# Performance work log

Hardware: AMD Instinct MI355X
Metric: run time of the kernel (lower is better)

Reference implementation:

```python
import jax, jax.numpy as jnp
import numpy as np

PROJ_DIM = 128
TEMP = 0.1
CLAMP_VAL = 50.0
EPS = 1e-6


def _coords(H, W):
    # [H*W, 2] grid of (x, y) coordinates, matching torch meshgrid indexing='ij'
    xs = jnp.arange(W, dtype=jnp.float32)
    ys = jnp.arange(H, dtype=jnp.float32)
    grid_y, grid_x = jnp.meshgrid(ys, xs, indexing='ij')
    return jnp.stack([grid_x.reshape(-1), grid_y.reshape(-1)], axis=-1)


def setup_inputs() -> dict:
    key = jax.random.key(0)
    k1, k2 = jax.random.split(key)
    B, C, H, W = 2, 128, 96, 96
    fL = jax.random.normal(k1, (B, C, H, W), dtype=jnp.float32)
    fR = jax.random.normal(k2, (B, C, H, W), dtype=jnp.float32)
    return {"fL": fL, "fR": fR}


def reference(fL, fR):
    B, C, H, W = fL.shape
    HW = H * W
    scale = jnp.float32(np.sqrt(PROJ_DIM))

    # L2-normalize over channel dim with epsilon clamp
    fLn = fL / jnp.maximum(jnp.linalg.norm(fL, axis=1, keepdims=True), EPS)
    fRn = fR / jnp.maximum(jnp.linalg.norm(fR, axis=1, keepdims=True), EPS)

    q = fLn.reshape(B, C, HW).transpose(0, 2, 1).astype(jnp.float32)  # [B, HW, C]
    k = fRn.reshape(B, C, HW).astype(jnp.float32)                      # [B, C, HW]

    coords = _coords(H, W)  # [HW, 2]

    # Global correlation: [B, HW, HW] (chunking in the original is math-equivalent)
    corr = jnp.einsum('bqc,bck->bqk', q, k) / scale
    corr = jnp.clip(corr / TEMP, -CLAMP_VAL, CLAMP_VAL)
    prob = jax.nn.softmax(corr, axis=-1)

    expected_pos = prob @ coords                 # [B, HW, 2]
    max_prob = jnp.max(prob, axis=-1)            # [B, HW]

    flow_abs = expected_pos.reshape(B, H, W, 2).transpose(0, 3, 1, 2)  # [B, 2, H, W]
    conf = max_prob.reshape(B, 1, H, W)

    src = coords.reshape(H, W, 2).transpose(2, 0, 1)[None]  # [1, 2, H, W]
    flow = (flow_abs - src).astype(fL.dtype)
    conf = conf.astype(fL.dtype)
    return flow, conf
```

## Files before the change

kernel.cpp:

```cpp
#include <hip/hip_runtime.h>
#include <stdint.h>

#define HW 9216
#define CDIM 128
#define WIDTH 96
#define BATCH 2
#define SPLITS 48
#define KSPLIT 192
#define NKG 6
#define QTILE 128
#define NQT (HW / QTILE)
#define NWG (NQT * SPLITS * BATCH)

#define QSCALE 0.44194173824159216f
#define MXSCALE 2.8853900817779268f

typedef _Float16 half8 __attribute__((ext_vector_type(8)));
typedef float f32x16 __attribute__((ext_vector_type(16)));
typedef float float2v __attribute__((ext_vector_type(2)));

__global__ __launch_bounds__(256) void norm_kernel(const float* __restrict__ fL,
                                                   const float* __restrict__ fR,
                                                   _Float16* __restrict__ Qh,
                                                   _Float16* __restrict__ Kh)
{
    __shared__ float ssred[4][64];
    __shared__ _Float16 ot[64 * 130];

    const float* src = (blockIdx.y == 0) ? fL : fR;
    _Float16* dst    = (blockIdx.y == 0) ? Qh : Kh;
    const float outScale = (blockIdx.y == 0) ? QSCALE : 1.0f;

    const int t = threadIdx.x;
    const int pos_l = t & 63, cg = t >> 6;
    const int pos0 = blockIdx.x * 64;
    const int b = pos0 / HW, pos_in = pos0 % HW + pos_l;

    const float* p = src + (size_t)b * CDIM * HW + pos_in;

    float v[32];
    float ss = 0.f;
    #pragma unroll
    for (int j = 0; j < 32; ++j) {
        v[j] = p[(size_t)(cg * 32 + j) * HW];
        ss += v[j] * v[j];
    }
    ssred[cg][pos_l] = ss;
    __syncthreads();
    float tot = ssred[0][pos_l] + ssred[1][pos_l] + ssred[2][pos_l] + ssred[3][pos_l];
    float scale = outScale / fmaxf(sqrtf(tot), 1e-6f);

    #pragma unroll
    for (int j = 0; j < 32; ++j)
        ot[pos_l * 130 + cg * 32 + j] = (_Float16)(v[j] * scale);
    __syncthreads();

    uint4* og = (uint4*)(dst + (size_t)(b * HW + pos0 % HW + 0) * CDIM);
    #pragma unroll
    for (int i = 0; i < 4; ++i) {
        int idx = i * 256 + t;
        int row = idx >> 4, chunk = idx & 15;
        og[idx] = *(const uint4*)&ot[row * 130 + chunk * 8];
    }
}

__global__ __launch_bounds__(256, 3) void attn_kernel(const _Float16* __restrict__ Qh,
                                                      const _Float16* __restrict__ Kh,
                                                      float4* __restrict__ part)
{
    __shared__ __align__(16) _Float16 Ks[KSPLIT * 128];

    const int wg0 = blockIdx.x;
    const int nid = (wg0 & 7) * (NWG / 8) + (wg0 >> 3);
    const int qt = nid % NQT;
    const int sb = nid / NQT;
    const int split = sb % SPLITS;
    const int b = sb / SPLITS;

    const int t = threadIdx.x;
    const int lane = t & 63, wave = t >> 6;
    const int lane31 = lane & 31, hi = lane >> 5;
    const int ln15 = lane & 15, qd = lane >> 4;

    const char* kp0 = (const char*)(Kh + (size_t)b * HW * CDIM) +
                      (size_t)(split * KSPLIT) * (CDIM * 2);

    {
        int voff4[4];
        #pragma unroll
        for (int i = 0; i < 4; ++i) {
            int r = wave * 48 + i * 4 + qd;
            voff4[i] = r * 256 + ((ln15 ^ (r & 15)) << 4) - i * 1024;
        }
        _Float16* db = &Ks[wave * (48 * 128)];
        #pragma unroll
        for (int i = 0; i < 12; ++i)
            __builtin_amdgcn_global_load_lds(
                (const __attribute__((address_space(1))) uint32_t*)(kp0 + voff4[i & 3] + i * 1024),
                (__attribute__((address_space(3))) uint32_t*)(db + i * 512),
                16, 0, 0);
    }

    half8 qf[8];
    {
        const char* qb = (const char*)(Qh +
            ((size_t)(b * HW + qt * QTILE + wave * 32 + lane31)) * CDIM);
        #pragma unroll
        for (int kc = 0; kc < 8; ++kc)
            qf[kc] = *(const half8*)(qb + kc * 32 + hi * 16);
    }

    int rdoff[8];
    #pragma unroll
    for (int kc = 0; kc < 8; ++kc)
        rdoff[kc] = (lane31 << 8) + ((((kc << 1) | hi) ^ ln15) << 4);

    const float ysp = (float)(split * 2);

    float2v E2[8];
    #pragma unroll
    for (int p = 0; p < 8; ++p) E2[p] = (float2v)0.f;
    float mxs = -1.0e30f;
    float2v axb2 = (float2v)0.f, ay2 = (float2v)0.f;

    const char* ksb = (const char*)&Ks[0];
    const float2v C4 = (float2v)(1.0f / 24.0f), C3 = (float2v)(1.0f / 6.0f),
                  C2 = (float2v)0.5f, C1 = (float2v)1.0f;

    __syncthreads();

    #define CHAIN2(ACCX, KGX, ACCY, KGY)                                         \
        {                                                                        \
            __builtin_amdgcn_s_setprio(1);                                       \
            _Pragma("unroll")                                                    \
            for (int kc = 0; kc < 8; ++kc) {                                     \
                half8 kx = *(const half8*)(ksb + (KGX) * 8192 + rdoff[kc]);      \
                half8 ky = *(const half8*)(ksb + (KGY) * 8192 + rdoff[kc]);      \
                ACCX = __builtin_amdgcn_mfma_f32_32x32x16_f16(                   \
                    kx, qf[kc], (kc == 0) ? (f32x16)0.f : ACCX, 0, 0, 0);        \
                ACCY = __builtin_amdgcn_mfma_f32_32x32x16_f16(                   \
                    ky, qf[kc], (kc == 0) ? (f32x16)0.f : ACCY, 0, 0, 0);        \
            }                                                                    \
            __builtin_amdgcn_s_setprio(0);                                       \
        }

    #define EPI(ACC, KG)                                                         \
        {                                                                        \
            const float xb = (float)(32 * ((KG) % 3));                           \
            const float yk = ysp + (float)((KG) / 3);                            \
            float2v lt2;                                                         \
            _Pragma("unroll")                                                    \
            for (int p = 0; p < 8; ++p) {                                        \
                float2v w;                                                       \
                w.x = ACC[2 * p];                                                \
                w.y = ACC[2 * p + 1];                                            \
                mxs = fmaxf(mxs, fmaxf(w.x, w.y));           \
                float2v h = w * C4 + C3;                       \
                h = h * w + C2;                                                  \
                h = h * w + C1;                                                  \
                h = h * w + C1;                                                  \
                float2v e = h * h;                                               \
                E2[p] += e;                                                      \
                lt2 = (p == 0) ? e : (lt2 + e);                                  \
            }                                                                    \
            axb2 += lt2 * (float2v)xb;                                           \
            ay2  += lt2 * (float2v)yk;                                           \
        }

    f32x16 accA, accB, accC, accD;
    CHAIN2(accA, 0, accB, 1)
    CHAIN2(accC, 2, accD, 3)
    __builtin_amdgcn_sched_barrier(0); EPI(accA, 0) EPI(accB, 1)
    CHAIN2(accA, 4, accB, 5)
    __builtin_amdgcn_sched_barrier(0); EPI(accC, 2) EPI(accD, 3)
    EPI(accA, 4) EPI(accB, 5)
    #undef CHAIN2
    #undef EPI

    float l = 0.f, axc = 0.f;
    #pragma unroll
    for (int p = 0; p < 8; ++p) {
        const float c0 = (float)(((2 * p) & 3) + 8 * ((2 * p) >> 2));
        l   += E2[p].x + E2[p].y;
        axc += c0 * E2[p].x + (c0 + 1.0f) * E2[p].y;
    }
    float ax = axc + (float)(4 * hi) * l + axb2.x + axb2.y;
    float ay = ay2.x + ay2.y;
    float mx = mxs;

    l  += __shfl_xor(l, 32, 64);
    ax += __shfl_xor(ax, 32, 64);
    ay += __shfl_xor(ay, 32, 64);
    mx  = fmaxf(mx, __shfl_xor(mx, 32, 64));

    if (hi == 0) {
        int row = qt * QTILE + wave * 32 + lane31;
        part[(size_t)split * (BATCH * HW) + b * HW + row] =
            make_float4(l, ax, ay, __builtin_amdgcn_exp2f(mx * MXSCALE));
    }
}

__global__ __launch_bounds__(256) void combine_kernel(const float4* __restrict__ part,
                                                      float* __restrict__ out)
{
    __shared__ float4 red[3][64];
    const int t = threadIdx.x;
    const int r = t & 63, g = t >> 6;
    const int tid = blockIdx.x * 64 + r;
    const int b = tid / HW, pos = tid % HW;

    float l = 0.f, ax = 0.f, ay = 0.f, mx = 0.f;
    #pragma unroll
    for (int s = 0; s < 12; ++s) {
        float4 v = part[(size_t)(g * 12 + s) * (BATCH * HW) + tid];
        l += v.x; ax += v.y; ay += v.z; mx = fmaxf(mx, v.w);
    }
    if (g > 0) red[g - 1][r] = make_float4(l, ax, ay, mx);
    __syncthreads();
    if (g == 0) {
        #pragma unroll
        for (int i = 0; i < 3; ++i) {
            float4 v = red[i][r];
            l += v.x; ax += v.y; ay += v.z; mx = fmaxf(mx, v.w);
        }
        float inv = 1.0f / l;
        int x = pos % WIDTH, y = pos / WIDTH;
        out[(size_t)b * 2 * HW + pos]                      = ax * inv - (float)x;
        out[(size_t)b * 2 * HW + HW + pos]                 = ay * inv - (float)y;
        out[(size_t)BATCH * 2 * HW + (size_t)b * HW + pos] = mx * inv;
    }
}

extern "C" void kernel_launch(void* const* d_in, const int* in_sizes, int n_in,
                              void* d_out, int out_size, void* d_ws, size_t ws_size,
                              hipStream_t stream)
{
    const float* fL = (const float*)d_in[0];
    const float* fR = (const float*)d_in[1];
    float* out = (float*)d_out;

    char* ws = (char*)d_ws;
    const size_t QH_BYTES = (size_t)BATCH * HW * CDIM * sizeof(_Float16);
    _Float16* Qh  = (_Float16*)ws;
    _Float16* Kh  = (_Float16*)(ws + QH_BYTES);
    float4*   part = (float4*)(ws + 2 * QH_BYTES);

    norm_kernel<<<dim3((BATCH * HW) / 64, 2), 256, 0, stream>>>(fL, fR, Qh, Kh);
    attn_kernel<<<dim3(NWG), 256, 0, stream>>>(Qh, Kh, part);
    combine_kernel<<<dim3((BATCH * HW) / 64), 256, 0, stream>>>(part, out);
}
```

Measured before the change: 141.7 us.

## Compute softmax-weighted coordinate sums with MFMA and hardware exp2

Replaces the quartic polynomial exp approximation with native exp2 by folding log2(e) into the query scale. The per-row sums of p, p*x and p*y now come from a second MFMA: the exponentials are packed to fp16 and multiplied against a constant matrix of ones, x coordinates and y coordinates. This moves the reduction work from VALU onto the matrix cores and removes the scalar epilogue. The cost is fp16 rounding of the probabilities and coordinates, a cross-lane shuffle to rearrange operands, and an LDS transpose with an extra block barrier.

```diff
diff --git a/kernel.cpp b/kernel.cpp
--- a/kernel.cpp
+++ b/kernel.cpp
@@ -12,12 +12,12 @@
 #define NQT (HW / QTILE)
 #define NWG (NQT * SPLITS * BATCH)
 
-#define QSCALE 0.44194173824159216f
-#define MXSCALE 2.8853900817779268f
+#define QSCALE 1.2753324954171245f
 
 typedef _Float16 half8 __attribute__((ext_vector_type(8)));
+typedef _Float16 half2v __attribute__((ext_vector_type(2)));
 typedef float f32x16 __attribute__((ext_vector_type(16)));
-typedef float float2v __attribute__((ext_vector_type(2)));
+typedef uint32_t u32x4 __attribute__((ext_vector_type(4)));
 
 __global__ __launch_bounds__(256) void norm_kernel(const float* __restrict__ fL,
                                                    const float* __restrict__ fR,
@@ -69,6 +69,7 @@
                                                       float4* __restrict__ part)
 {
     __shared__ __align__(16) _Float16 Ks[KSPLIT * 128];
+    __shared__ float tr[4][3][32];
 
     const int wg0 = blockIdx.x;
     const int nid = (wg0 & 7) * (NWG / 8) + (wg0 >> 3);
@@ -116,87 +117,111 @@
         rdoff[kc] = (lane31 << 8) + ((((kc << 1) | hi) ^ ln15) << 4);
 
     const float ysp = (float)(split * 2);
-
-    float2v E2[8];
-    #pragma unroll
-    for (int p = 0; p < 8; ++p) E2[p] = (float2v)0.f;
+    half8 Bv[3][2];
+    {
+        const int col = lane31;
+        const uint32_t onepk = 0x3C003C00u;
+        uint32_t ypk = __builtin_bit_cast(uint32_t,
+                           __builtin_amdgcn_cvt_pkrtz(ysp, ysp));
+        #pragma unroll
+        for (int ph = 0; ph < 3; ++ph)
+            #pragma unroll
+            for (int m = 0; m < 2; ++m) {
+                u32x4 bb;
+                #pragma unroll
+                for (int jj = 0; jj < 4; ++jj) {
+                    float x0 = (float)(32 * ph + m * 16 + hi * 8 + 2 * jj);
+                    uint32_t xpk = __builtin_bit_cast(uint32_t,
+                                       __builtin_amdgcn_cvt_pkrtz(x0, x0 + 1.f));
+                    bb[jj] = (col == 0) ? onepk : (col == 1) ? xpk
+                           : (col == 2) ? ypk : 0u;
+                }
+                Bv[ph][m] = __builtin_bit_cast(half8, bb);
+            }
+    }
+
+    f32x16 pv = (f32x16)0.f;
     float mxs = -1.0e30f;
-    float2v axb2 = (float2v)0.f, ay2 = (float2v)0.f;
 
     const char* ksb = (const char*)&Ks[0];
-    const float2v C4 = (float2v)(1.0f / 24.0f), C3 = (float2v)(1.0f / 6.0f),
-                  C2 = (float2v)0.5f, C1 = (float2v)1.0f;
-
-    __syncthreads();
-
-    #define CHAIN2(ACCX, KGX, ACCY, KGY)                                         \
+
+    __syncthreads();
+
+    #define CHAIN(ACC, KG)                                                       \
         {                                                                        \
             __builtin_amdgcn_s_setprio(1);                                       \
             _Pragma("unroll")                                                    \
             for (int kc = 0; kc < 8; ++kc) {                                     \
-                half8 kx = *(const half8*)(ksb + (KGX) * 8192 + rdoff[kc]);      \
-                half8 ky = *(const half8*)(ksb + (KGY) * 8192 + rdoff[kc]);      \
-                ACCX = __builtin_amdgcn_mfma_f32_32x32x16_f16(                   \
-                    kx, qf[kc], (kc == 0) ? (f32x16)0.f : ACCX, 0, 0, 0);        \
-                ACCY = __builtin_amdgcn_mfma_f32_32x32x16_f16(                   \
-                    ky, qf[kc], (kc == 0) ? (f32x16)0.f : ACCY, 0, 0, 0);        \
+                half8 kf = *(const half8*)(ksb + (KG) * 8192 + rdoff[kc]);       \
+                ACC = __builtin_amdgcn_mfma_f32_32x32x16_f16(                    \
+                    kf, qf[kc], (kc == 0) ? (f32x16)0.f : ACC, 0, 0, 0);         \
             }                                                                    \
             __builtin_amdgcn_s_setprio(0);                                       \
         }
 
-    #define EPI(ACC, KG)                                                         \
+    #define EPI(ACC, PH)                                                         \
         {                                                                        \
-            const float xb = (float)(32 * ((KG) % 3));                           \
-            const float yk = ysp + (float)((KG) / 3);                            \
-            float2v lt2;                                                         \
+            uint32_t ep[8], sw[8];                                               \
             _Pragma("unroll")                                                    \
             for (int p = 0; p < 8; ++p) {                                        \
-                float2v w;                                                       \
-                w.x = ACC[2 * p];                                                \
-                w.y = ACC[2 * p + 1];                                            \
-                mxs = fmaxf(mxs, fmaxf(w.x, w.y));           \
-                float2v h = w * C4 + C3;                       \
-                h = h * w + C2;                                                  \
-                h = h * w + C1;                                                  \
-                h = h * w + C1;                                                  \
-                float2v e = h * h;                                               \
-                E2[p] += e;                                                      \
-                lt2 = (p == 0) ? e : (lt2 + e);                                  \
+                float wx = ACC[2 * p], wy = ACC[2 * p + 1];                      \
+                mxs = fmaxf(mxs, fmaxf(wx, wy));                                 \
+                float ex = __builtin_amdgcn_exp2f(wx);                           \
+                float ey = __builtin_amdgcn_exp2f(wy);                           \
+                ep[p] = __builtin_bit_cast(uint32_t,                             \
+                            __builtin_amdgcn_cvt_pkrtz(ex, ey));                 \
             }                                                                    \
-            axb2 += lt2 * (float2v)xb;                                           \
-            ay2  += lt2 * (float2v)yk;                                           \
-        }
-
-    f32x16 accA, accB, accC, accD;
-    CHAIN2(accA, 0, accB, 1)
-    CHAIN2(accC, 2, accD, 3)
-    __builtin_amdgcn_sched_barrier(0); EPI(accA, 0) EPI(accB, 1)
-    CHAIN2(accA, 4, accB, 5)
-    __builtin_amdgcn_sched_barrier(0); EPI(accC, 2) EPI(accD, 3)
-    EPI(accA, 4) EPI(accB, 5)
-    #undef CHAIN2
+            _Pragma("unroll")                                                    \
+            for (int p = 0; p < 8; ++p)                                          \
+                sw[p] = (uint32_t)__shfl_xor((int)ep[p], 32, 64);                \
+            u32x4 a1, a2;                                                        \
+            a1[0] = hi ? sw[2] : ep[0]; a1[1] = hi ? sw[3] : ep[1];              \
+            a1[2] = hi ? ep[2] : sw[0]; a1[3] = hi ? ep[3] : sw[1];              \
+            a2[0] = hi ? sw[6] : ep[4]; a2[1] = hi ? sw[7] : ep[5];              \
+            a2[2] = hi ? ep[6] : sw[4]; a2[3] = hi ? ep[7] : sw[5];              \
+            pv = __builtin_amdgcn_mfma_f32_32x32x16_f16(                         \
+                     __builtin_bit_cast(half8, a1), Bv[PH][0], pv, 0, 0, 0);     \
+            pv = __builtin_amdgcn_mfma_f32_32x32x16_f16(                         \
+                     __builtin_bit_cast(half8, a2), Bv[PH][1], pv, 0, 0, 0);     \
+        }
+
+    f32x16 accA, accB;
+    CHAIN(accA, 0)
+    CHAIN(accB, 1) __builtin_amdgcn_sched_barrier(0); EPI(accA, 0)
+    CHAIN(accA, 2) __builtin_amdgcn_sched_barrier(0); EPI(accB, 1)
+    CHAIN(accB, 3) __builtin_amdgcn_sched_barrier(0); EPI(accA, 2)
+    {
+        const _Float16 dyv = (lane31 == 2) ? (_Float16)1.0f : (_Float16)0.0f;
+        half8 dy8 = { dyv, dyv, dyv, dyv, dyv, dyv, dyv, dyv };
+        #pragma unroll
+        for (int ph = 0; ph < 3; ++ph)
+            #pragma unroll
+            for (int m = 0; m < 2; ++m)
+                Bv[ph][m] += dy8;
+    }
+    CHAIN(accA, 4) __builtin_amdgcn_sched_barrier(0); EPI(accB, 0)
+    CHAIN(accB, 5) __builtin_amdgcn_sched_barrier(0); EPI(accA, 1)
+    EPI(accB, 2)
+    #undef CHAIN
     #undef EPI
 
-    float l = 0.f, axc = 0.f;
-    #pragma unroll
-    for (int p = 0; p < 8; ++p) {
-        const float c0 = (float)(((2 * p) & 3) + 8 * ((2 * p) >> 2));
-        l   += E2[p].x + E2[p].y;
-        axc += c0 * E2[p].x + (c0 + 1.0f) * E2[p].y;
-    }
-    float ax = axc + (float)(4 * hi) * l + axb2.x + axb2.y;
-    float ay = ay2.x + ay2.y;
-    float mx = mxs;
-
-    l  += __shfl_xor(l, 32, 64);
-    ax += __shfl_xor(ax, 32, 64);
-    ay += __shfl_xor(ay, 32, 64);
-    mx  = fmaxf(mx, __shfl_xor(mx, 32, 64));
+    if (lane31 < 3) {
+        #pragma unroll
+        for (int r = 0; r < 16; ++r) {
+            int qp = (r & 3) + 8 * (r >> 2) + 4 * hi;
+            tr[wave][lane31][qp] = pv[r];
+        }
+    }
+    float mx = fmaxf(mxs, __shfl_xor(mxs, 32, 64));
+    __syncthreads();
 
     if (hi == 0) {
+        float l  = tr[wave][0][lane31];
+        float ax = tr[wave][1][lane31];
+        float ay = tr[wave][2][lane31];
         int row = qt * QTILE + wave * 32 + lane31;
         part[(size_t)split * (BATCH * HW) + b * HW + row] =
-            make_float4(l, ax, ay, __builtin_amdgcn_exp2f(mx * MXSCALE));
+            make_float4(l, ax, ay, __builtin_amdgcn_exp2f(mx));
     }
 }
 
```

After: 289.2 us. 104% more time.
